# Optimization experiments

Hardware: AMD Instinct MI355X
Metric: run time of the kernel (lower is better)

Reference implementation:

```python
import jax, jax.numpy as jnp
import numpy as np

N_USERS = 100000
N_ITEMS = 200000
N_NODES = N_USERS + N_ITEMS
LATENT_DIM = 64
N_LAYERS = 3
NNZ = 6400000


def setup_inputs() -> dict:
    key = jax.random.key(0)
    k1, k2, k3, k4, k5 = jax.random.split(key, 5)
    user_emb = 0.1 * jax.random.normal(k1, (N_USERS, LATENT_DIM), dtype=jnp.float32)
    item_emb = 0.1 * jax.random.normal(k2, (N_ITEMS, LATENT_DIM), dtype=jnp.float32)
    rows = jax.random.randint(k3, (NNZ,), 0, N_NODES, dtype=jnp.int32)
    cols = jax.random.randint(k4, (NNZ,), 0, N_NODES, dtype=jnp.int32)
    # normalized-adjacency-like positive values
    vals = jax.random.uniform(k5, (NNZ,), dtype=jnp.float32) * 0.05
    return {"user_emb": user_emb, "item_emb": item_emb,
            "rows": rows, "cols": cols, "vals": vals}


def _spmm(rows, cols, vals, x):
    # y[r] += vals[e] * x[cols[e]]  for each edge e with rows[e]==r
    gathered = vals[:, None] * x[cols]          # [nnz, D]
    return jax.ops.segment_sum(gathered, rows, num_segments=N_NODES)


def reference(user_emb, item_emb, rows, cols, vals):
    # LightGCN.computer(): multi-hop propagation + layer mean pooling
    all_emb = jnp.concatenate([user_emb, item_emb], axis=0)   # [N, D]
    acc = all_emb
    for _ in range(N_LAYERS):
        all_emb = _spmm(rows, cols, vals, all_emb)
        acc = acc + all_emb
    light_out = acc / (N_LAYERS + 1)
    users = light_out[:N_USERS]
    items = light_out[N_USERS:]
    return users, items
```

## Files before the change

kernel.cpp:

```cpp
#include <hip/hip_runtime.h>
#include <hip/hip_bf16.h>

#define N_USERS 100000
#define N_ITEMS 200000
#define N_NODES 300000
#define DIM 64

#define TOT_ELEMS ((size_t)N_NODES * DIM)
#define TOT_F4    (TOT_ELEMS / 4)
#define USER_F4   (((size_t)N_USERS * DIM) / 4)

#define BROWS 512
#define NBUCKET ((N_NODES + BROWS - 1) / BROWS)
#define EPT 32
#define EDGES_PER_BLOCK (EPT * 256)

typedef float        f4_native __attribute__((ext_vector_type(4)));
typedef unsigned int u4_native __attribute__((ext_vector_type(4)));

__device__ __forceinline__ float bf2f(unsigned short u) {
    return __uint_as_float((unsigned int)u << 16);
}
__device__ __forceinline__ unsigned short f2bf(float f) {
    __hip_bfloat16 h = __float2bfloat16(f);
    return *reinterpret_cast<unsigned short*>(&h);
}
__device__ __forceinline__ float lo_bf(unsigned int u) {
    return __uint_as_float(u << 16);
}
__device__ __forceinline__ float hi_bf(unsigned int u) {
    return __uint_as_float(u & 0xFFFF0000u);
}

__global__ void init_kernel(const float* __restrict__ user,
                            const float* __restrict__ item,
                            ushort4* __restrict__ xh) {
    size_t i = (size_t)blockIdx.x * blockDim.x + threadIdx.x;
    if (i >= TOT_F4) return;
    f4_native v = (i < USER_F4)
        ? __builtin_nontemporal_load((const f4_native*)user + i)
        : __builtin_nontemporal_load((const f4_native*)item + (i - USER_F4));
    ushort4 h;
    h.x = f2bf(v.x); h.y = f2bf(v.y); h.z = f2bf(v.z); h.w = f2bf(v.w);
    xh[i] = h;
}

__global__ void zero_buckets_kernel(int* __restrict__ bucket_count) {
    int i = blockIdx.x * blockDim.x + threadIdx.x;
    if (i < NBUCKET) bucket_count[i] = 0;
}

__global__ void bucket_hist_kernel(const int* __restrict__ rows,
                                   int* __restrict__ bucket_count, int nnz) {
    __shared__ int h[NBUCKET];
    int t = threadIdx.x;
    size_t base = (size_t)blockIdx.x * EDGES_PER_BLOCK;
    for (int i = t; i < NBUCKET; i += 256) h[i] = 0;
    __syncthreads();
    #pragma unroll 4
    for (int k = 0; k < EPT; ++k) {
        size_t e = base + (size_t)k * 256 + t;
        if (e < (size_t)nnz) atomicAdd(&h[rows[e] >> 9], 1);
    }
    __syncthreads();
    for (int i = t; i < NBUCKET; i += 256) {
        int c = h[i];
        if (c) atomicAdd(&bucket_count[i], c);
    }
}

__global__ void bucket_scan_kernel(const int* __restrict__ bucket_count,
                                   int* __restrict__ bucket_base,
                                   int* __restrict__ bucket_cursor, int nnz) {
    __shared__ int s[1024];
    int t = threadIdx.x;
    int orig = (t < NBUCKET) ? bucket_count[t] : 0;
    s[t] = orig;
    __syncthreads();
    for (int off = 1; off < 1024; off <<= 1) {
        int v = (t >= off) ? s[t - off] : 0;
        __syncthreads();
        s[t] += v;
        __syncthreads();
    }
    if (t < NBUCKET) {
        int excl = s[t] - orig;
        bucket_base[t]   = excl;
        bucket_cursor[t] = excl;
    }
    if (t == 0) bucket_base[NBUCKET] = nnz;
}

__global__ void binA_kernel(const int* __restrict__ rows,
                            const int* __restrict__ cols,
                            const float* __restrict__ vals,
                            int* __restrict__ bucket_cursor,
                            int2* __restrict__ binned,
                            int nnz) {
    __shared__ int  h[NBUCKET];
    __shared__ int  lstart[NBUCKET];
    __shared__ int  lcur[NBUCKET];
    __shared__ int  gbase[NBUCKET];
    __shared__ int  s[256];
    __shared__ int2 ledge[EDGES_PER_BLOCK];

    int t = threadIdx.x;
    size_t base = (size_t)blockIdx.x * EDGES_PER_BLOCK;
    int nvalid = (int)(((size_t)nnz - base < (size_t)EDGES_PER_BLOCK)
                       ? ((size_t)nnz - base) : (size_t)EDGES_PER_BLOCK);

    for (int i = t; i < NBUCKET; i += 256) h[i] = 0;
    __syncthreads();

    #pragma unroll 4
    for (int k = 0; k < EPT; ++k) {
        int e = k * 256 + t;
        if (e < nvalid) atomicAdd(&h[rows[base + e] >> 9], 1);
    }
    __syncthreads();

    int i0 = 3 * t, i1 = 3 * t + 1, i2 = 3 * t + 2;
    int c0 = (i0 < NBUCKET) ? h[i0] : 0;
    int c1 = (i1 < NBUCKET) ? h[i1] : 0;
    int c2 = (i2 < NBUCKET) ? h[i2] : 0;
    int g = c0 + c1 + c2;
    s[t] = g;
    __syncthreads();
    for (int off = 1; off < 256; off <<= 1) {
        int v = (t >= off) ? s[t - off] : 0;
        __syncthreads();
        s[t] += v;
        __syncthreads();
    }
    int excl = s[t] - g;
    if (i0 < NBUCKET) { lstart[i0] = excl;           lcur[i0] = excl; }
    if (i1 < NBUCKET) { lstart[i1] = excl + c0;      lcur[i1] = excl + c0; }
    if (i2 < NBUCKET) { lstart[i2] = excl + c0 + c1; lcur[i2] = excl + c0 + c1; }

    for (int i = t; i < NBUCKET; i += 256) {
        int c = h[i];
        gbase[i] = c ? atomicAdd(&bucket_cursor[i], c) : 0;
    }
    __syncthreads();

    #pragma unroll 4
    for (int k = 0; k < EPT; ++k) {
        int e = k * 256 + t;
        if (e < nvalid) {
            size_t ge = base + e;
            int r = rows[ge];
            int c = __builtin_nontemporal_load(cols + ge);
            float v = __builtin_nontemporal_load(vals + ge);
            int slot = atomicAdd(&lcur[r >> 9], 1);
            ledge[slot] = make_int2(((r & (BROWS - 1)) << 19) | c,
                                    __float_as_int(v));
        }
    }
    __syncthreads();

    for (int slot = t; slot < nvalid; slot += 256) {
        int lo = 0, hi = NBUCKET;
        while (hi - lo > 1) {
            int mid = (lo + hi) >> 1;
            if (lstart[mid] <= slot) lo = mid; else hi = mid;
        }
        binned[gbase[lo] + (slot - lstart[lo])] = ledge[slot];
    }
}

__global__ void binB_kernel(const int* __restrict__ bucket_base,
                            const int2* __restrict__ binned,
                            int2* __restrict__ sorted,
                            int* __restrict__ row_ptr,
                            int nnz) {
    __shared__ int cnt[BROWS];
    __shared__ int cur[BROWS];
    __shared__ int s[256];
    int b = blockIdx.x, t = threadIdx.x;
    int beg = bucket_base[b];
    int end = bucket_base[b + 1];
    int row0 = b * BROWS;
    for (int i = t; i < BROWS; i += 256) cnt[i] = 0;
    __syncthreads();
    for (int idx = beg + t; idx < end; idx += 256) {
        int lr = ((unsigned)binned[idx].x) >> 19;
        atomicAdd(&cnt[lr], 1);
    }
    __syncthreads();
    int c0 = cnt[2 * t], c1 = cnt[2 * t + 1];
    int local = c0 + c1;
    s[t] = local;
    __syncthreads();
    for (int off = 1; off < 256; off <<= 1) {
        int v = (t >= off) ? s[t - off] : 0;
        __syncthreads();
        s[t] += v;
        __syncthreads();
    }
    int excl = beg + s[t] - local;
    int r0 = row0 + 2 * t;
    if (r0 < N_NODES)     row_ptr[r0]     = excl;
    if (r0 + 1 < N_NODES) row_ptr[r0 + 1] = excl + c0;
    cur[2 * t]     = excl;
    cur[2 * t + 1] = excl + c0;
    __syncthreads();
    for (int idx = beg + t; idx < end; idx += 256) {
        int2 e = binned[idx];
        int lr  = ((unsigned)e.x) >> 19;
        int col = e.x & 0x7FFFF;
        int pos = atomicAdd(&cur[lr], 1);
        sorted[pos] = make_int2(col, e.y);
    }
    if (b == 0 && t == 0) row_ptr[N_NODES] = nnz;
}

__device__ __forceinline__ void row_accum8(int beg, int end, int l,
                                           const int2* __restrict__ sorted,
                                           const unsigned short* __restrict__ srch,
                                           float* acc) {
    const int e7   = l & 7;
    const int idxb = (l & ~7) << 2;
    const uint4* __restrict__ src4 = (const uint4*)srch;

    int len = end - beg;
    int m = len;
    m = max(m, __shfl_xor(m, 8));
    m = max(m, __shfl_xor(m, 16));
    m = max(m, __shfl_xor(m, 32));
    int nb = (m + 7) >> 3;
    if (nb <= 0) return;

    int cc = 0, vc = 0;
    {
        int e = beg + e7;
        if (e < end) {
            unsigned long long ed = __builtin_nontemporal_load(
                (const unsigned long long*)sorted + e);
            cc = (int)(unsigned int)(ed & 0xFFFFFFFFull);
            vc = (int)(unsigned int)(ed >> 32);
        }
    }
    for (int b = 0; b < nb; ++b) {
        int cn = 0, vn = 0;
        if (b + 1 < nb) {
            int e = beg + ((b + 1) << 3) + e7;
            if (e < end) {
                unsigned long long ed = __builtin_nontemporal_load(
                    (const unsigned long long*)sorted + e);
                cn = (int)(unsigned int)(ed & 0xFFFFFFFFull);
                vn = (int)(unsigned int)(ed >> 32);
            }
        }
        #pragma unroll
        for (int j = 0; j < 8; ++j) {
            int   c = __builtin_amdgcn_ds_bpermute(idxb + (j << 2), cc);
            float v = __int_as_float(__builtin_amdgcn_ds_bpermute(idxb + (j << 2), vc));
            uint4 u = src4[(size_t)(((unsigned)c << 3) | (unsigned)e7)];
            acc[0] = fmaf(v, lo_bf(u.x), acc[0]);
            acc[1] = fmaf(v, hi_bf(u.x), acc[1]);
            acc[2] = fmaf(v, lo_bf(u.y), acc[2]);
            acc[3] = fmaf(v, hi_bf(u.y), acc[3]);
            acc[4] = fmaf(v, lo_bf(u.z), acc[4]);
            acc[5] = fmaf(v, hi_bf(u.z), acc[5]);
            acc[6] = fmaf(v, lo_bf(u.w), acc[6]);
            acc[7] = fmaf(v, hi_bf(u.w), acc[7]);
        }
        cc = cn; vc = vn;
    }
}

__global__ void spmm_row_kernel(const int* __restrict__ row_ptr,
                                const int2* __restrict__ sorted,
                                const unsigned short* __restrict__ srch,
                                unsigned short* __restrict__ dsth) {
    int t = blockIdx.x * blockDim.x + threadIdx.x;
    int w = t >> 6;
    int l = t & 63;
    int r = w * 8 + (l >> 3);
    if (r >= N_NODES) return;
    float acc[8] = {0.f, 0.f, 0.f, 0.f, 0.f, 0.f, 0.f, 0.f};
    row_accum8(row_ptr[r], row_ptr[r + 1], l, sorted, srch, acc);
    uint4 o;
    o.x = (unsigned)f2bf(acc[0]) | ((unsigned)f2bf(acc[1]) << 16);
    o.y = (unsigned)f2bf(acc[2]) | ((unsigned)f2bf(acc[3]) << 16);
    o.z = (unsigned)f2bf(acc[4]) | ((unsigned)f2bf(acc[5]) << 16);
    o.w = (unsigned)f2bf(acc[6]) | ((unsigned)f2bf(acc[7]) << 16);
    ((uint4*)dsth)[(size_t)r * 8 + (l & 7)] = o;
}

__global__ void spmm_final_kernel(const int* __restrict__ row_ptr,
                                  const int2* __restrict__ sorted,
                                  const unsigned short* __restrict__ y2h,
                                  const unsigned short* __restrict__ y1h,
                                  const float* __restrict__ user,
                                  const float* __restrict__ item,
                                  float* __restrict__ out) {
    int t = blockIdx.x * blockDim.x + threadIdx.x;
    int w = t >> 6;
    int l = t & 63;
    int r = w * 8 + (l >> 3);
    if (r >= N_NODES) return;
    float acc[8] = {0.f, 0.f, 0.f, 0.f, 0.f, 0.f, 0.f, 0.f};
    row_accum8(row_ptr[r], row_ptr[r + 1], l, sorted, y2h, acc);

    int e7 = l & 7;
    size_t q4 = (size_t)r * 8 + e7;
    u4_native y1q = __builtin_nontemporal_load((const u4_native*)y1h + q4);
    u4_native y2q = __builtin_nontemporal_load((const u4_native*)y2h + q4);
    size_t fidx = (size_t)r * 16 + 2 * e7;
    const f4_native* bp = (r < N_USERS)
        ? ((const f4_native*)user + fidx)
        : ((const f4_native*)item + (fidx - (size_t)N_USERS * 16));
    f4_native b0 = __builtin_nontemporal_load(bp);
    f4_native b1 = __builtin_nontemporal_load(bp + 1);
    f4_native o0, o1;
    o0.x = 0.25f * (b0.x + lo_bf(y1q.x) + lo_bf(y2q.x) + acc[0]);
    o0.y = 0.25f * (b0.y + hi_bf(y1q.x) + hi_bf(y2q.x) + acc[1]);
    o0.z = 0.25f * (b0.z + lo_bf(y1q.y) + lo_bf(y2q.y) + acc[2]);
    o0.w = 0.25f * (b0.w + hi_bf(y1q.y) + hi_bf(y2q.y) + acc[3]);
    o1.x = 0.25f * (b1.x + lo_bf(y1q.z) + lo_bf(y2q.z) + acc[4]);
    o1.y = 0.25f * (b1.y + hi_bf(y1q.z) + hi_bf(y2q.z) + acc[5]);
    o1.z = 0.25f * (b1.z + lo_bf(y1q.w) + lo_bf(y2q.w) + acc[6]);
    o1.w = 0.25f * (b1.w + hi_bf(y1q.w) + hi_bf(y2q.w) + acc[7]);
    __builtin_nontemporal_store(o0, (f4_native*)out + fidx);
    __builtin_nontemporal_store(o1, (f4_native*)out + fidx + 1);
}

extern "C" void kernel_launch(void* const* d_in, const int* in_sizes, int n_in,
                              void* d_out, int out_size, void* d_ws, size_t ws_size,
                              hipStream_t stream) {
    const float* user = (const float*)d_in[0];
    const float* item = (const float*)d_in[1];
    const int*   rows = (const int*)d_in[2];
    const int*   cols = (const int*)d_in[3];
    const float* vals = (const float*)d_in[4];
    int nnz = in_sizes[2];

    float* out = (float*)d_out;

    char* p = (char*)d_ws;
    unsigned short* xh  = (unsigned short*)p; p += TOT_ELEMS * 2;
    unsigned short* y1h = (unsigned short*)p; p += TOT_ELEMS * 2;
    unsigned short* y2h = (unsigned short*)p; p += TOT_ELEMS * 2;
    int2* binned = (int2*)p; p += (size_t)nnz * sizeof(int2);
    int2* sorted = (int2*)p; p += (size_t)nnz * sizeof(int2);
    int* row_ptr       = (int*)p; p += (size_t)(N_NODES + 1) * 4;
    int* bucket_count  = (int*)p; p += (size_t)NBUCKET * 4;
    int* bucket_base   = (int*)p; p += (size_t)(NBUCKET + 1) * 4;
    int* bucket_cursor = (int*)p; p += (size_t)NBUCKET * 4;

    const int BLK = 256;
    int grid_elem = (int)((TOT_F4 + BLK - 1) / BLK);
    int grid_binA = (nnz + EDGES_PER_BLOCK - 1) / EDGES_PER_BLOCK;
    int grid_spmm = (int)(((size_t)(N_NODES / 8) * 64 + BLK - 1) / BLK);

    init_kernel<<<grid_elem, BLK, 0, stream>>>(user, item, (ushort4*)xh);

    zero_buckets_kernel<<<(NBUCKET + BLK - 1) / BLK, BLK, 0, stream>>>(bucket_count);
    bucket_hist_kernel<<<grid_binA, BLK, 0, stream>>>(rows, bucket_count, nnz);
    bucket_scan_kernel<<<1, 1024, 0, stream>>>(bucket_count, bucket_base, bucket_cursor, nnz);

    binA_kernel<<<grid_binA, BLK, 0, stream>>>(rows, cols, vals, bucket_cursor, binned, nnz);
    binB_kernel<<<NBUCKET, BLK, 0, stream>>>(bucket_base, binned, sorted, row_ptr, nnz);

    spmm_row_kernel<<<grid_spmm, BLK, 0, stream>>>(row_ptr, sorted, xh,  y1h);
    spmm_row_kernel<<<grid_spmm, BLK, 0, stream>>>(row_ptr, sorted, y1h, y2h);
    spmm_final_kernel<<<grid_spmm, BLK, 0, stream>>>(row_ptr, sorted, y2h, y1h,
                                                     user, item, out);
}
```

Measured before the change: 786.6 us.

## Reorder rows by degree bucket to balance work within SpMM wavefronts

Adds a counting sort of rows by edge-block count (histogram, scan, scatter) to produce a row permutation. The SpMM kernels then process rows in this order, so the eight rows sharing a wavefront have similar lengths and fewer lanes idle waiting on the longest row. This adds four small preprocessing kernels, an extra indirection load per row, and non-sequential output writes.

```diff
diff --git a/kernel.cpp b/kernel.cpp
--- a/kernel.cpp
+++ b/kernel.cpp
@@ -14,6 +14,7 @@
 #define NBUCKET ((N_NODES + BROWS - 1) / BROWS)
 #define EPT 32
 #define EDGES_PER_BLOCK (EPT * 256)
+#define NBB 64
 
 typedef float        f4_native __attribute__((ext_vector_type(4)));
 typedef unsigned int u4_native __attribute__((ext_vector_type(4)));
@@ -214,6 +215,90 @@
     if (b == 0 && t == 0) row_ptr[N_NODES] = nnz;
 }
 
+__global__ void zero_nb_kernel(int* __restrict__ nb_count) {
+    int i = threadIdx.x;
+    if (i < NBB) nb_count[i] = 0;
+}
+
+__global__ void nb_hist_kernel(const int* __restrict__ row_ptr,
+                               int* __restrict__ nb_count) {
+    __shared__ int h[NBB];
+    int b = blockIdx.x, t = threadIdx.x;
+    int row0 = b * BROWS;
+    if (t < NBB) h[t] = 0;
+    __syncthreads();
+    #pragma unroll
+    for (int k = 0; k < 2; ++k) {
+        int r = row0 + k * 256 + t;
+        if (r < N_NODES) {
+            int len = row_ptr[r + 1] - row_ptr[r];
+            int nb = (len + 7) >> 3;
+            if (nb > NBB - 1) nb = NBB - 1;
+            atomicAdd(&h[nb], 1);
+        }
+    }
+    __syncthreads();
+    if (t < NBB) {
+        int c = h[t];
+        if (c) atomicAdd(&nb_count[t], c);
+    }
+}
+
+__global__ void nb_scan_kernel(const int* __restrict__ nb_count,
+                               int* __restrict__ nb_cursor) {
+    __shared__ int s[NBB];
+    int t = threadIdx.x;
+    int orig = nb_count[t];
+    s[t] = orig;
+    __syncthreads();
+    for (int off = 1; off < NBB; off <<= 1) {
+        int v = (t >= off) ? s[t - off] : 0;
+        __syncthreads();
+        s[t] += v;
+        __syncthreads();
+    }
+    nb_cursor[t] = s[t] - orig;
+}
+
+__global__ void degree_bin_kernel(const int* __restrict__ row_ptr,
+                                  int* __restrict__ nb_cursor,
+                                  int* __restrict__ row_order) {
+    __shared__ int h[NBB];
+    __shared__ int gb[NBB];
+    int b = blockIdx.x, t = threadIdx.x;
+    int row0 = b * BROWS;
+    if (t < NBB) h[t] = 0;
+    __syncthreads();
+    #pragma unroll
+    for (int k = 0; k < 2; ++k) {
+        int r = row0 + k * 256 + t;
+        if (r < N_NODES) {
+            int len = row_ptr[r + 1] - row_ptr[r];
+            int nb = (len + 7) >> 3;
+            if (nb > NBB - 1) nb = NBB - 1;
+            atomicAdd(&h[nb], 1);
+        }
+    }
+    __syncthreads();
+    if (t < NBB) {
+        int c = h[t];
+        gb[t] = c ? atomicAdd(&nb_cursor[t], c) : 0;
+        h[t] = 0;
+    }
+    __syncthreads();
+    #pragma unroll
+    for (int k = 0; k < 2; ++k) {
+        int r = row0 + k * 256 + t;
+        if (r < N_NODES) {
+            int len = row_ptr[r + 1] - row_ptr[r];
+            int nb = (len + 7) >> 3;
+            if (nb > NBB - 1) nb = NBB - 1;
+            int pos = gb[nb] + atomicAdd(&h[nb], 1);
+            row_order[pos] = r;
+        }
+    }
+}
+
 __device__ __forceinline__ void row_accum8(int beg, int end, int l,
                                            const int2* __restrict__ sorted,
                                            const unsigned short* __restrict__ srch,
@@ -270,14 +355,16 @@
 }
 
 __global__ void spmm_row_kernel(const int* __restrict__ row_ptr,
+                                const int* __restrict__ row_order,
                                 const int2* __restrict__ sorted,
                                 const unsigned short* __restrict__ srch,
                                 unsigned short* __restrict__ dsth) {
     int t = blockIdx.x * blockDim.x + threadIdx.x;
     int w = t >> 6;
     int l = t & 63;
-    int r = w * 8 + (l >> 3);
-    if (r >= N_NODES) return;
+    int ri = w * 8 + (l >> 3);
+    if (ri >= N_NODES) return;
+    int r = row_order[ri];
     float acc[8] = {0.f, 0.f, 0.f, 0.f, 0.f, 0.f, 0.f, 0.f};
     row_accum8(row_ptr[r], row_ptr[r + 1], l, sorted, srch, acc);
     uint4 o;
@@ -289,6 +376,7 @@
 }
 
 __global__ void spmm_final_kernel(const int* __restrict__ row_ptr,
+                                  const int* __restrict__ row_order,
                                   const int2* __restrict__ sorted,
                                   const unsigned short* __restrict__ y2h,
                                   const unsigned short* __restrict__ y1h,
@@ -298,8 +386,9 @@
     int t = blockIdx.x * blockDim.x + threadIdx.x;
     int w = t >> 6;
     int l = t & 63;
-    int r = w * 8 + (l >> 3);
-    if (r >= N_NODES) return;
+    int ri = w * 8 + (l >> 3);
+    if (ri >= N_NODES) return;
+    int r = row_order[ri];
     float acc[8] = {0.f, 0.f, 0.f, 0.f, 0.f, 0.f, 0.f, 0.f};
     row_accum8(row_ptr[r], row_ptr[r + 1], l, sorted, y2h, acc);
 
@@ -349,6 +438,10 @@
     int* bucket_base   = (int*)p; p += (size_t)(NBUCKET + 1) * 4;
     int* bucket_cursor = (int*)p; p += (size_t)NBUCKET * 4;
 
+    int* row_order = (int*)binned;
+    int* nb_count  = (int*)binned + N_NODES;
+    int* nb_cursor = (int*)binned + N_NODES + NBB;
+
     const int BLK = 256;
     int grid_elem = (int)((TOT_F4 + BLK - 1) / BLK);
     int grid_binA = (nnz + EDGES_PER_BLOCK - 1) / EDGES_PER_BLOCK;
@@ -363,8 +456,13 @@
     binA_kernel<<<grid_binA, BLK, 0, stream>>>(rows, cols, vals, bucket_cursor, binned, nnz);
     binB_kernel<<<NBUCKET, BLK, 0, stream>>>(bucket_base, binned, sorted, row_ptr, nnz);
 
-    spmm_row_kernel<<<grid_spmm, BLK, 0, stream>>>(row_ptr, sorted, xh,  y1h);
-    spmm_row_kernel<<<grid_spmm, BLK, 0, stream>>>(row_ptr, sorted, y1h, y2h);
-    spmm_final_kernel<<<grid_spmm, BLK, 0, stream>>>(row_ptr, sorted, y2h, y1h,
+    zero_nb_kernel<<<1, NBB, 0, stream>>>(nb_count);
+    nb_hist_kernel<<<NBUCKET, BLK, 0, stream>>>(row_ptr, nb_count);
+    nb_scan_kernel<<<1, NBB, 0, stream>>>(nb_count, nb_cursor);
+    degree_bin_kernel<<<NBUCKET, BLK, 0, stream>>>(row_ptr, nb_cursor, row_order);
+
+    spmm_row_kernel<<<grid_spmm, BLK, 0, stream>>>(row_ptr, row_order, sorted, xh,  y1h);
+    spmm_row_kernel<<<grid_spmm, BLK, 0, stream>>>(row_ptr, row_order, sorted, y1h, y2h);
+    spmm_final_kernel<<<grid_spmm, BLK, 0, stream>>>(row_ptr, row_order, sorted, y2h, y1h,
                                                      user, item, out);
 }
```

Result: slower. 828.0 us (+5.3%).
